# Optimization experiments

Measured on AMD Instinct MI355X. Metric: run time of the kernel, lower is better.

Reference implementation:

```python
import jax, jax.numpy as jnp
import numpy as np

N1, N2, D = 8192, 8192, 128

def setup_inputs() -> dict:
    key = jax.random.key(0)
    k1, k2, k3, k4 = jax.random.split(key, 4)
    X1 = jax.random.normal(k1, (N1, D), dtype=jnp.float32)
    X2 = jax.random.normal(k2, (N2, D), dtype=jnp.float32)
    task1 = jax.random.randint(k3, (N1,), 0, 2, dtype=jnp.int32)
    task2 = jax.random.randint(k4, (N2,), 0, 2, dtype=jnp.int32)
    # learned parameters (init values match module defaults: lengthscale=1, output_variance=1, b=0)
    log_l = jnp.zeros((D,), dtype=jnp.float32)          # log(1)
    log_theta_l = jnp.zeros((1,), dtype=jnp.float32)    # log(1)
    b = jnp.zeros((1,), dtype=jnp.float32)
    return {"X1": X1, "X2": X2, "log_l": log_l, "log_theta_l": log_theta_l,
            "b": b, "task1": task1, "task2": task2}

def reference(X1, X2, log_l, log_theta_l, b, task1, task2):
    l = jnp.exp(log_l)                      # (D,) ARD lengthscales
    A = X1 / l                              # (N1, D)
    B = X2 / l                              # (N2, D)
    # sum((a-b)^2) = |a|^2 + |b|^2 - 2 a.b  -> GEMM form, no (N1,N2,D) intermediate
    sq_dist = (jnp.sum(A * A, axis=1)[:, None]
               + jnp.sum(B * B, axis=1)[None, :]
               - 2.0 * (A @ B.T))
    sq_dist = jnp.maximum(sq_dist, 0.0)
    K_base = jnp.exp(log_theta_l[0]) * jnp.exp(-0.5 * sq_dist)   # (N1, N2)
    # lambda = clip(2/(1+exp(b)) - 1, 0, 1)
    lam = jnp.clip(2.0 / (1.0 + jnp.exp(b[0])) - 1.0, 0.0, 1.0)
    diff_task = task1[:, None] != task2[None, :]                 # (N1, N2) bool
    K = K_base * jnp.where(diff_task, lam, 1.0)
    return K
```

## Files before the change

kernel.cpp:

```cpp
#include <hip/hip_runtime.h>
#include <stdint.h>

typedef float f32x4 __attribute__((ext_vector_type(4)));
typedef int   i32x4 __attribute__((ext_vector_type(4)));
typedef __bf16 bf16x8 __attribute__((ext_vector_type(8)));

#define NN 8192
#define DDIM 128
#define RSTRIDE 80

#define OFF_AH 0
#define OFF_AL 10240
#define OFF_BH 20480
#define OFF_BL 30720
#define OFF_ILS 40960
#define OFF_N1  41472
#define OFF_N2  41984
#define LDS_TOT 42496

__device__ __forceinline__ uint32_t pk2(__bf16 a, __bf16 b) {
    return (uint32_t)__builtin_bit_cast(unsigned short, a)
         | ((uint32_t)__builtin_bit_cast(unsigned short, b) << 16);
}

__device__ __forceinline__ void split4(f32x4 x, uint2& hi, uint2& lo) {
    __bf16 h0 = (__bf16)x[0], h1 = (__bf16)x[1], h2 = (__bf16)x[2], h3 = (__bf16)x[3];
    hi.x = pk2(h0, h1); hi.y = pk2(h2, h3);
    __bf16 l0 = (__bf16)(x[0] - (float)h0);
    __bf16 l1 = (__bf16)(x[1] - (float)h1);
    __bf16 l2 = (__bf16)(x[2] - (float)h2);
    __bf16 l3 = (__bf16)(x[3] - (float)h3);
    lo.x = pk2(l0, l1); lo.y = pk2(l2, l3);
}

__device__ __forceinline__ void lds_barrier() {
    asm volatile("s_waitcnt lgkmcnt(0)" ::: "memory");
    __builtin_amdgcn_sched_barrier(0);
    __builtin_amdgcn_s_barrier();
    __builtin_amdgcn_sched_barrier(0);
}

__global__ __launch_bounds__(256, 3) void tgp_kernel(
    const float* __restrict__ X1, const float* __restrict__ X2,
    const float* __restrict__ log_l,
    const float* __restrict__ log_theta_l, const float* __restrict__ bparam,
    const int* __restrict__ task1, const int* __restrict__ task2,
    float* __restrict__ C)
{
    __shared__ __align__(16) char smem[LDS_TOT];
    float* const ils = (float*)(smem + OFF_ILS);
    float* const n1s = (float*)(smem + OFF_N1);
    float* const n2s = (float*)(smem + OFF_N2);

    const int t = threadIdx.x;
    const int lane = t & 63;
    const int wv = t >> 6;
    const int wr = wv >> 1, wc = wv & 1;
    const int lr = lane & 15, lg = lane >> 4;
    const int kq = t & 7;
    const int rg = t >> 3;

    int wg = blockIdx.x;
    int xcd = wg & 7;
    int r = wg >> 3;
    int su = r >> 6;
    int inner = r & 63;
    int tm = xcd * 8 + (inner >> 3);
    int tn = su * 8 + (inner & 7);

    const float* Ag = X1 + (size_t)tm * 128 * DDIM;
    const float* Bg = X2 + (size_t)tn * 128 * DDIM;

    if (t < 128) ils[t] = __expf(-log_l[t]);

    f32x4 aV[4], bV[4];
    #pragma unroll
    for (int e = 0; e < 4; ++e) {
        aV[e] = *(const f32x4*)(Ag + (size_t)(e * 32 + rg) * DDIM + kq * 4);
        bV[e] = *(const f32x4*)(Bg + (size_t)(e * 32 + rg) * DDIM + kq * 4);
    }
    __syncthreads();

    float nA[4] = {0.f, 0.f, 0.f, 0.f};
    float nB[4] = {0.f, 0.f, 0.f, 0.f};
    f32x4 acc[4][4];
    #pragma unroll
    for (int i = 0; i < 4; ++i)
        #pragma unroll
        for (int j = 0; j < 4; ++j) acc[i][j] = (f32x4){0.f, 0.f, 0.f, 0.f};

    for (int c = 0; c < 4; ++c) {
        f32x4 il4 = *(const f32x4*)(ils + c * 32 + kq * 4);
        #pragma unroll
        for (int e = 0; e < 4; ++e) {
            int rr = e * 32 + rg;
            f32x4 xa = aV[e] * il4;
            f32x4 xb = bV[e] * il4;
            nA[e] += xa[0]*xa[0] + xa[1]*xa[1] + xa[2]*xa[2] + xa[3]*xa[3];
            nB[e] += xb[0]*xb[0] + xb[1]*xb[1] + xb[2]*xb[2] + xb[3]*xb[3];
            uint2 hA, lA, hB, lB;
            split4(xa, hA, lA);
            split4(xb, hB, lB);
            int boff = rr * RSTRIDE + kq * 8;
            *(uint2*)(smem + OFF_AH + boff) = hA;
            *(uint2*)(smem + OFF_AL + boff) = lA;
            *(uint2*)(smem + OFF_BH + boff) = hB;
            *(uint2*)(smem + OFF_BL + boff) = lB;
        }
        if (c < 3) {
            #pragma unroll
            for (int e = 0; e < 4; ++e) {
                aV[e] = *(const f32x4*)(Ag + (size_t)(e * 32 + rg) * DDIM + (c + 1) * 32 + kq * 4);
                bV[e] = *(const f32x4*)(Bg + (size_t)(e * 32 + rg) * DDIM + (c + 1) * 32 + kq * 4);
            }
        }
        lds_barrier();

        {
            bf16x8 ah[4], bh[4], xf[4];
            #pragma unroll
            for (int mi = 0; mi < 4; ++mi) {
                int off = (wr * 64 + mi * 16 + lr) * RSTRIDE + lg * 16;
                ah[mi] = *(const bf16x8*)(smem + OFF_AH + off);
            }
            #pragma unroll
            for (int ni = 0; ni < 4; ++ni) {
                int off = (wc * 64 + ni * 16 + lr) * RSTRIDE + lg * 16;
                bh[ni] = *(const bf16x8*)(smem + OFF_BH + off);
            }
            #pragma unroll
            for (int mi = 0; mi < 4; ++mi)
                #pragma unroll
                for (int ni = 0; ni < 4; ++ni)
                    acc[mi][ni] = __builtin_amdgcn_mfma_f32_16x16x32_bf16(bh[ni], ah[mi], acc[mi][ni], 0, 0, 0);
            #pragma unroll
            for (int mi = 0; mi < 4; ++mi) {
                int off = (wr * 64 + mi * 16 + lr) * RSTRIDE + lg * 16;
                xf[mi] = *(const bf16x8*)(smem + OFF_AL + off);
            }
            #pragma unroll
            for (int mi = 0; mi < 4; ++mi)
                #pragma unroll
                for (int ni = 0; ni < 4; ++ni)
                    acc[mi][ni] = __builtin_amdgcn_mfma_f32_16x16x32_bf16(bh[ni], xf[mi], acc[mi][ni], 0, 0, 0);
            #pragma unroll
            for (int ni = 0; ni < 4; ++ni) {
                int off = (wc * 64 + ni * 16 + lr) * RSTRIDE + lg * 16;
                xf[ni] = *(const bf16x8*)(smem + OFF_BL + off);
            }
            #pragma unroll
            for (int mi = 0; mi < 4; ++mi)
                #pragma unroll
                for (int ni = 0; ni < 4; ++ni)
                    acc[mi][ni] = __builtin_amdgcn_mfma_f32_16x16x32_bf16(xf[ni], ah[mi], acc[mi][ni], 0, 0, 0);
        }
        lds_barrier();
    }

    #pragma unroll
    for (int e = 0; e < 4; ++e) {
        #pragma unroll
        for (int off = 1; off < 8; off <<= 1) {
            nA[e] += __shfl_xor(nA[e], off);
            nB[e] += __shfl_xor(nB[e], off);
        }
    }
    if ((t & 7) == 0) {
        #pragma unroll
        for (int e = 0; e < 4; ++e) {
            n1s[e * 32 + rg] = nA[e];
            n2s[e * 32 + rg] = nB[e];
        }
    }
    __syncthreads();

    float logt = log_theta_l[0];
    float bb = bparam[0];
    float lam = fminf(fmaxf(2.f / (1.f + __expf(bb)) - 1.f, 0.f), 1.f);
    int rbase = tm * 128, cbase = tn * 128;

    #pragma unroll
    for (int mi = 0; mi < 4; ++mi) {
        int rowl = wr * 64 + mi * 16 + lr;
        float n1v = n1s[rowl];
        int t1v = task1[rbase + rowl];
        #pragma unroll
        for (int ni = 0; ni < 4; ++ni) {
            int coll = wc * 64 + ni * 16 + lg * 4;
            f32x4 n2v = *(const f32x4*)(n2s + coll);
            i32x4 t2v = *(const i32x4*)(task2 + cbase + coll);
            f32x4 kv;
            #pragma unroll
            for (int rix = 0; rix < 4; ++rix) {
                float s = fmaxf(n1v + n2v[rix] - 2.f * acc[mi][ni][rix], 0.f);
                float k = __expf(fmaf(-0.5f, s, logt));
                kv[rix] = (t1v != t2v[rix]) ? k * lam : k;
            }
            *(f32x4*)(C + (size_t)(rbase + rowl) * NN + cbase + coll) = kv;
        }
    }
}

extern "C" void kernel_launch(void* const* d_in, const int* in_sizes, int n_in,
                              void* d_out, int out_size, void* d_ws, size_t ws_size,
                              hipStream_t stream)
{
    const float* X1 = (const float*)d_in[0];
    const float* X2 = (const float*)d_in[1];
    const float* log_l = (const float*)d_in[2];
    const float* log_theta = (const float*)d_in[3];
    const float* bp = (const float*)d_in[4];
    const int* t1 = (const int*)d_in[5];
    const int* t2 = (const int*)d_in[6];
    float* C = (float*)d_out;
    (void)d_ws; (void)ws_size; (void)in_sizes; (void)n_in; (void)out_size;

    tgp_kernel<<<4096, 256, 0, stream>>>(X1, X2, log_l, log_theta, bp, t1, t2, C);
}
```

Baseline: 98.62 us.

## Precompute scaled bf16 hi/lo operands into output scratch, stream via global_load_lds

```diff
diff --git a/kernel.cpp b/kernel.cpp
--- a/kernel.cpp
+++ b/kernel.cpp
@@ -7,21 +7,170 @@
 
 #define NN 8192
 #define DDIM 128
-#define RSTRIDE 80
-
-#define OFF_AH 0
-#define OFF_AL 10240
-#define OFF_BH 20480
-#define OFF_BL 30720
-#define OFF_ILS 40960
-#define OFF_N1  41472
-#define OFF_N2  41984
-#define LDS_TOT 42496
+
+#define APRIME_OFF 0u
+#define BPRIME_OFF (8192u*512u)
+#define NORM_OFF   (268435456u - 65536u)
 
 __device__ __forceinline__ uint32_t pk2(__bf16 a, __bf16 b) {
     return (uint32_t)__builtin_bit_cast(unsigned short, a)
          | ((uint32_t)__builtin_bit_cast(unsigned short, b) << 16);
 }
+
+__device__ __forceinline__ void gload_lds16(const void* g, void* l) {
+    __builtin_amdgcn_global_load_lds(
+        (const __attribute__((address_space(1))) uint32_t*)g,
+        (__attribute__((address_space(3))) uint32_t*)l,
+        16, 0, 0);
+}
+
+__global__ __launch_bounds__(256) void prep_kernel(
+    const float* __restrict__ X1, const float* __restrict__ X2,
+    const float* __restrict__ log_l, char* __restrict__ outbuf)
+{
+    int t = threadIdx.x, wave = t >> 6, lane = t & 63;
+    int row = blockIdx.x * 4 + wave;
+    const float* X; uint32_t base; float* nrm;
+    if (row < NN) {
+        X = X1 + (size_t)row * DDIM;
+        base = APRIME_OFF + (uint32_t)row * 512u;
+        nrm = (float*)(outbuf + NORM_OFF) + row;
+    } else {
+        int r2 = row - NN;
+        X = X2 + (size_t)r2 * DDIM;
+        base = BPRIME_OFF + (uint32_t)r2 * 512u;
+        nrm = (float*)(outbuf + NORM_OFF) + NN + r2;
+    }
+    int c0 = lane * 2;
+    float2 x = *(const float2*)(X + c0);
+    float a0 = x.x * __expf(-log_l[c0]);
+    float a1 = x.y * __expf(-log_l[c0 + 1]);
+    float ss = a0 * a0 + a1 * a1;
+    #pragma unroll
+    for (int o = 32; o; o >>= 1) ss += __shfl_down(ss, o);
+    if (lane == 0) *nrm = ss;
+    __bf16 h0 = (__bf16)a0, h1 = (__bf16)a1;
+    __bf16 l0 = (__bf16)(a0 - (float)h0), l1 = (__bf16)(a1 - (float)h1);
+    int j = lane >> 2;
+    int phys = (j & 8) | ((j & 7) ^ (row & 7));
+    uint32_t off = base + (uint32_t)phys * 16u + (uint32_t)(lane & 3) * 4u;
+    *(uint32_t*)(outbuf + off)        = pk2(h0, h1);
+    *(uint32_t*)(outbuf + off + 256u) = pk2(l0, l1);
+}
+
+__global__ __launch_bounds__(256, 3) void fast_kernel(
+    const char* __restrict__ stash,
+    const int* __restrict__ task1, const int* __restrict__ task2,
+    const float* __restrict__ log_theta_l, const float* __restrict__ bparam,
+    float* __restrict__ C)
+{
+    __shared__ __align__(16) char smem[32768];
+    const int t = threadIdx.x;
+    const int lane = t & 63, wv = t >> 6;
+    const int wr = wv >> 1, wc = wv & 1;
+    const int lr = lane & 15, lg = lane >> 4;
+
+    int wg = blockIdx.x;
+    int swz = (wg & 7) * 488 + (wg >> 3);
+    int tm = 2 + (swz >> 6);
+    int tn = swz & 63;
+
+    const char* Abase = stash + APRIME_OFF + (size_t)tm * 128 * 512;
+    const char* Bbase = stash + BPRIME_OFF + (size_t)tn * 128 * 512;
+
+    f32x4 acc[4][4];
+    #pragma unroll
+    for (int i = 0; i < 4; ++i)
+        #pragma unroll
+        for (int j = 0; j < 4; ++j) acc[i][j] = (f32x4){0.f, 0.f, 0.f, 0.f};
+
+    #define STAGE(c) do {                                                         \
+        _Pragma("unroll")                                                         \
+        for (int i = 0; i < 4; ++i) {                                             \
+            int l = t + i * 256;                                                  \
+            gload_lds16(Abase + (size_t)(l >> 3) * 512 + (c) * 128 + (l & 7) * 16,\
+                        smem + l * 16);                                           \
+            gload_lds16(Bbase + (size_t)(l >> 3) * 512 + (c) * 128 + (l & 7) * 16,\
+                        smem + 16384 + l * 16);                                   \
+        }                                                                         \
+    } while (0)
+
+    #define FRAGMM() do {                                                         \
+        _Pragma("unroll")                                                         \
+        for (int ks = 0; ks < 2; ++ks) {                                          \
+            bf16x8 af[4], bfr[4];                                                 \
+            _Pragma("unroll")                                                     \
+            for (int mi = 0; mi < 4; ++mi) {                                      \
+                int row = wr * 64 + mi * 16 + lr;                                 \
+                af[mi] = *(const bf16x8*)(smem + row * 128                        \
+                          + (((ks * 4 + lg) ^ (row & 7)) * 16));                  \
+            }                                                                     \
+            _Pragma("unroll")                                                     \
+            for (int ni = 0; ni < 4; ++ni) {                                      \
+                int row = wc * 64 + ni * 16 + lr;                                 \
+                bfr[ni] = *(const bf16x8*)(smem + 16384 + row * 128               \
+                          + (((ks * 4 + lg) ^ (row & 7)) * 16));                  \
+            }                                                                     \
+            _Pragma("unroll")                                                     \
+            for (int mi = 0; mi < 4; ++mi)                                        \
+                _Pragma("unroll")                                                 \
+                for (int ni = 0; ni < 4; ++ni)                                    \
+                    acc[mi][ni] = __builtin_amdgcn_mfma_f32_16x16x32_bf16(        \
+                        bfr[ni], af[mi], acc[mi][ni], 0, 0, 0);                   \
+        }                                                                         \
+    } while (0)
+
+    STAGE(0);
+    __syncthreads();
+    FRAGMM();
+    #pragma unroll
+    for (int c = 1; c < 4; ++c) {
+        __syncthreads();
+        STAGE(c);
+        __syncthreads();
+        FRAGMM();
+    }
+
+    const float* n1g = (const float*)(stash + NORM_OFF);
+    const float* n2g = n1g + NN;
+    float logt = log_theta_l[0];
+    float bb = bparam[0];
+    float lam = fminf(fmaxf(2.f / (1.f + __expf(bb)) - 1.f, 0.f), 1.f);
+    int rbase = tm * 128, cbase = tn * 128;
+
+    #pragma unroll
+    for (int mi = 0; mi < 4; ++mi) {
+        int rowl = wr * 64 + mi * 16 + lr;
+        float n1v = n1g[rbase + rowl];
+        int t1v = task1[rbase + rowl];
+        #pragma unroll
+        for (int ni = 0; ni < 4; ++ni) {
+            int coll = wc * 64 + ni * 16 + lg * 4;
+            f32x4 n2v = *(const f32x4*)(n2g + cbase + coll);
+            i32x4 t2v = *(const i32x4*)(task2 + cbase + coll);
+            f32x4 kv;
+            #pragma unroll
+            for (int rix = 0; rix < 4; ++rix) {
+                float s = fmaxf(n1v + n2v[rix] - 2.f * acc[mi][ni][rix], 0.f);
+                float k = __expf(fmaf(-0.5f, s, logt));
+                kv[rix] = (t1v != t2v[rix]) ? k * lam : k;
+            }
+            *(f32x4*)(C + (size_t)(rbase + rowl) * NN + cbase + coll) = kv;
+        }
+    }
+    #undef STAGE
+    #undef FRAGMM
+}
+
+#define RSTRIDE 80
+#define S_AH 0
+#define S_AL 10240
+#define S_BH 20480
+#define S_BL 30720
+#define S_ILS 40960
+#define S_N1  41472
+#define S_N2  41984
+#define S_TOT 42496
 
 __device__ __forceinline__ void split4(f32x4 x, uint2& hi, uint2& lo) {
     __bf16 h0 = (__bf16)x[0], h1 = (__bf16)x[1], h2 = (__bf16)x[2], h3 = (__bf16)x[3];
@@ -40,17 +189,17 @@
     __builtin_amdgcn_sched_barrier(0);
 }
 
-__global__ __launch_bounds__(256, 3) void tgp_kernel(
+__global__ __launch_bounds__(256, 3) void slow_kernel(
     const float* __restrict__ X1, const float* __restrict__ X2,
     const float* __restrict__ log_l,
     const float* __restrict__ log_theta_l, const float* __restrict__ bparam,
     const int* __restrict__ task1, const int* __restrict__ task2,
     float* __restrict__ C)
 {
-    __shared__ __align__(16) char smem[LDS_TOT];
-    float* const ils = (float*)(smem + OFF_ILS);
-    float* const n1s = (float*)(smem + OFF_N1);
-    float* const n2s = (float*)(smem + OFF_N2);
+    __shared__ __align__(16) char smem[S_TOT];
+    float* const ils = (float*)(smem + S_ILS);
+    float* const n1s = (float*)(smem + S_N1);
+    float* const n2s = (float*)(smem + S_N2);
 
     const int t = threadIdx.x;
     const int lane = t & 63;
@@ -61,12 +210,9 @@
     const int rg = t >> 3;
 
     int wg = blockIdx.x;
-    int xcd = wg & 7;
-    int r = wg >> 3;
-    int su = r >> 6;
-    int inner = r & 63;
-    int tm = xcd * 8 + (inner >> 3);
-    int tn = su * 8 + (inner & 7);
+    int tsel = wg >> 6;
+    int tm = (tsel == 2) ? 63 : tsel;
+    int tn = wg & 63;
 
     const float* Ag = X1 + (size_t)tm * 128 * DDIM;
     const float* Bg = X2 + (size_t)tn * 128 * DDIM;
@@ -90,22 +236,24 @@
         for (int j = 0; j < 4; ++j) acc[i][j] = (f32x4){0.f, 0.f, 0.f, 0.f};
 
     for (int c = 0; c < 4; ++c) {
-        f32x4 il4 = *(const f32x4*)(ils + c * 32 + kq * 4);
-        #pragma unroll
-        for (int e = 0; e < 4; ++e) {
-            int rr = e * 32 + rg;
-            f32x4 xa = aV[e] * il4;
-            f32x4 xb = bV[e] * il4;
-            nA[e] += xa[0]*xa[0] + xa[1]*xa[1] + xa[2]*xa[2] + xa[3]*xa[3];
-            nB[e] += xb[0]*xb[0] + xb[1]*xb[1] + xb[2]*xb[2] + xb[3]*xb[3];
-            uint2 hA, lA, hB, lB;
-            split4(xa, hA, lA);
-            split4(xb, hB, lB);
-            int boff = rr * RSTRIDE + kq * 8;
-            *(uint2*)(smem + OFF_AH + boff) = hA;
-            *(uint2*)(smem + OFF_AL + boff) = lA;
-            *(uint2*)(smem + OFF_BH + boff) = hB;
-            *(uint2*)(smem + OFF_BL + boff) = lB;
+        {
+            f32x4 il4 = *(const f32x4*)(ils + c * 32 + kq * 4);
+            #pragma unroll
+            for (int e = 0; e < 4; ++e) {
+                int rr = e * 32 + rg;
+                f32x4 xa = aV[e] * il4;
+                f32x4 xb = bV[e] * il4;
+                nA[e] += xa[0]*xa[0] + xa[1]*xa[1] + xa[2]*xa[2] + xa[3]*xa[3];
+                nB[e] += xb[0]*xb[0] + xb[1]*xb[1] + xb[2]*xb[2] + xb[3]*xb[3];
+                uint2 hA, lA, hB, lB;
+                split4(xa, hA, lA);
+                split4(xb, hB, lB);
+                int boff = rr * RSTRIDE + kq * 8;
+                *(uint2*)(smem + S_AH + boff) = hA;
+                *(uint2*)(smem + S_AL + boff) = lA;
+                *(uint2*)(smem + S_BH + boff) = hB;
+                *(uint2*)(smem + S_BL + boff) = lB;
+            }
         }
         if (c < 3) {
             #pragma unroll
@@ -115,18 +263,17 @@
             }
         }
         lds_barrier();
-
         {
             bf16x8 ah[4], bh[4], xf[4];
             #pragma unroll
             for (int mi = 0; mi < 4; ++mi) {
                 int off = (wr * 64 + mi * 16 + lr) * RSTRIDE + lg * 16;
-                ah[mi] = *(const bf16x8*)(smem + OFF_AH + off);
+                ah[mi] = *(const bf16x8*)(smem + S_AH + off);
             }
             #pragma unroll
             for (int ni = 0; ni < 4; ++ni) {
                 int off = (wc * 64 + ni * 16 + lr) * RSTRIDE + lg * 16;
-                bh[ni] = *(const bf16x8*)(smem + OFF_BH + off);
+                bh[ni] = *(const bf16x8*)(smem + S_BH + off);
             }
             #pragma unroll
             for (int mi = 0; mi < 4; ++mi)
@@ -136,7 +283,7 @@
             #pragma unroll
             for (int mi = 0; mi < 4; ++mi) {
                 int off = (wr * 64 + mi * 16 + lr) * RSTRIDE + lg * 16;
-                xf[mi] = *(const bf16x8*)(smem + OFF_AL + off);
+                xf[mi] = *(const bf16x8*)(smem + S_AL + off);
             }
             #pragma unroll
             for (int mi = 0; mi < 4; ++mi)
@@ -146,7 +293,7 @@
             #pragma unroll
             for (int ni = 0; ni < 4; ++ni) {
                 int off = (wc * 64 + ni * 16 + lr) * RSTRIDE + lg * 16;
-                xf[ni] = *(const bf16x8*)(smem + OFF_BL + off);
+                xf[ni] = *(const bf16x8*)(smem + S_BL + off);
             }
             #pragma unroll
             for (int mi = 0; mi < 4; ++mi)
@@ -165,7 +312,7 @@
             nB[e] += __shfl_xor(nB[e], off);
         }
     }
-    if ((t & 7) == 0) {
+    if (kq == 0) {
         #pragma unroll
         for (int e = 0; e < 4; ++e) {
             n1s[e * 32 + rg] = nA[e];
@@ -215,5 +362,7 @@
     float* C = (float*)d_out;
     (void)d_ws; (void)ws_size; (void)in_sizes; (void)n_in; (void)out_size;
 
-    tgp_kernel<<<4096, 256, 0, stream>>>(X1, X2, log_l, log_theta, bp, t1, t2, C);
-}
+    prep_kernel<<<4096, 256, 0, stream>>>(X1, X2, log_l, (char*)d_out);
+    fast_kernel<<<3904, 256, 0, stream>>>((const char*)d_out, t1, t2, log_theta, bp, C);
+    slow_kernel<<<192, 256, 0, stream>>>(X1, X2, log_l, log_theta, bp, t1, t2, C);
+}
```

After: 95.21 us. 3.5% less time.
